# Kernel tuning notes

Measured on AMD Instinct MI355X. Metric: run time of the kernel, lower is better.

Reference implementation:

```python
import jax, jax.numpy as jnp
import numpy as np

B, S, D = 4, 1024, 1024
H, HD = 16, 64
MAXPOS = 1024  # max_position_embeddings


def setup_inputs() -> dict:
    key = jax.random.key(0)
    ks = jax.random.split(key, 10)
    sc = 0.02
    return {
        "hidden_states": jax.random.normal(ks[0], (B, S, D), dtype=jnp.float32),
        "attention_mask": jnp.zeros((B, 1, 1, S), dtype=jnp.float32),
        "across_attention_prior": jax.random.uniform(ks[1], (B, H, S, S), dtype=jnp.float32),
        "head_mask": jnp.ones((1, H, 1, 1), dtype=jnp.float32),
        "Wq": jax.random.normal(ks[2], (D, D), dtype=jnp.float32) * sc,
        "bq": jnp.zeros((D,), dtype=jnp.float32),
        "Wk": jax.random.normal(ks[3], (D, D), dtype=jnp.float32) * sc,
        "bk": jnp.zeros((D,), dtype=jnp.float32),
        "Wv": jax.random.normal(ks[4], (D, D), dtype=jnp.float32) * sc,
        "bv": jnp.zeros((D,), dtype=jnp.float32),
        "dist_emb": jax.random.normal(ks[5], (2 * MAXPOS - 1, HD), dtype=jnp.float32) * sc,
    }


def _heads(x):
    # [B,S,D] -> [B,H,S,HD]
    return x.reshape(B, S, H, HD).transpose(0, 2, 1, 3)


def reference(hidden_states, attention_mask, across_attention_prior, head_mask,
              Wq, bq, Wk, bk, Wv, bv, dist_emb):
    q = _heads(hidden_states @ Wq + bq)  # [B,H,S,HD]
    k = _heads(hidden_states @ Wk + bk)
    v = _heads(hidden_states @ Wv + bv)

    scores = jnp.einsum("bhld,bhrd->bhlr", q, k)

    # relative_key_query positional bias
    pos = jnp.arange(S)
    distance = pos[:, None] - pos[None, :]  # [S,S]
    pe = dist_emb[distance + MAXPOS - 1]  # [S,S,HD] (l, r, d)
    scores = scores + jnp.einsum("bhld,lrd->bhlr", q, pe)
    scores = scores + jnp.einsum("bhrd,lrd->bhlr", k, pe)

    scores = scores / jnp.sqrt(jnp.float32(HD))
    scores = scores + attention_mask  # additive mask, broadcast [B,1,1,S]

    probs = jax.nn.softmax(scores, axis=-1)
    probs = probs * across_attention_prior  # post-softmax multiplicative prior
    probs = probs * head_mask  # dropout prob = 0 (eval)

    ctx = jnp.einsum("bhlr,bhrd->bhld", probs, v)
    ctx = ctx.transpose(0, 2, 1, 3).reshape(B, S, D)
    return ctx
```

## Files before the change

kernel.cpp:

```cpp
#include <hip/hip_runtime.h>


typedef unsigned short u16;
typedef unsigned int   u32;
typedef unsigned long long u64;
typedef __attribute__((ext_vector_type(8))) short bfx8;
typedef __attribute__((ext_vector_type(4))) float f32x4;

#define MFMA_BF16(a, b, c) __builtin_amdgcn_mfma_f32_16x16x32_bf16(a, b, c, 0, 0, 0)

__device__ __forceinline__ u16 f2bf(float f) {
    union { float f; u32 u; } c; c.f = f;
    u32 u = c.u;
    return (u16)((u + 0x7FFFu + ((u >> 16) & 1u)) >> 16);
}
__device__ __forceinline__ float bf2f(u16 v) {
    union { u32 u; float f; } c; c.u = ((u32)v) << 16;
    return c.f;
}
__device__ __forceinline__ float load_f(const void* p, long i, bool bf) {
    return bf ? bf2f(((const u16*)p)[i]) : ((const float*)p)[i];
}
__device__ __forceinline__ u16 load_bf(const void* p, long i, bool bf) {
    return bf ? ((const u16*)p)[i] : f2bf(((const float*)p)[i]);
}

__device__ __forceinline__ void gload16(const u16* g, u16* l) {
    __builtin_amdgcn_global_load_lds(
        (__attribute__((address_space(1))) void*)g,
        (__attribute__((address_space(3))) void*)l, 16, 0, 0);
}

__device__ __forceinline__ bfx8 ld_sw(const u16* arr, int row, int chunk) {
    return *(const bfx8*)(arr + row * 64 + ((chunk ^ (row & 7)) * 8));
}

__global__ void k_detect(const u32* hid, int* flags) {
    __shared__ int cnt;
    if (threadIdx.x == 0) cnt = 0;
    __syncthreads();
    int c = 0;
    for (int i = threadIdx.x; i < 1024; i += 256) {
        u32 w = hid[i];
        u32 e = (w >> 7) & 0xFFu;
        if (e >= 100u && e <= 140u) c++;
    }
    atomicAdd(&cnt, c);
    __syncthreads();
    if (threadIdx.x == 0) flags[0] = (cnt > 512) ? 1 : 0;
}

__global__ void k_prep(const void* hidden, const void* dist, const void* mask,
                       const void* hm, const void* bq, const void* bk,
                       const void* bv, const int* flags, u16* hid_bf,
                       u16* dist_bf, float* mask_f, float* hm_f, float* bias_f) {
    const bool bf = flags[0] != 0;
    const long NH = 4L * 1024 * 1024, ND = 2047L * 64, NM = 4096, NB = 3072, NHM = 16;
    const long TOT = NH + ND + NM + NB + NHM;
    for (long i = (long)blockIdx.x * 256 + threadIdx.x; i < TOT;
         i += (long)gridDim.x * 256) {
        if (i < NH) hid_bf[i] = load_bf(hidden, i, bf);
        else if (i < NH + ND) dist_bf[i - NH] = load_bf(dist, i - NH, bf);
        else if (i < NH + ND + NM) mask_f[i - NH - ND] = load_f(mask, i - NH - ND, bf);
        else if (i < NH + ND + NM + NB) {
            long j = i - NH - ND - NM;
            const void* src = (j < 1024) ? bq : ((j < 2048) ? bk : bv);
            bias_f[j] = load_f(src, j & 1023, bf);
        } else {
            long j = i - NH - ND - NM - NB;
            hm_f[j] = load_f(hm, j, bf);
        }
    }
}

__global__ void k_transpose(const void* Wq, const void* Wk, const void* Wv,
                            const int* flags, u16* wt) {
    const bool bf = flags[0] != 0;
    __shared__ float t[32][33];
    const int z = blockIdx.z;
    const void* W = (z == 0) ? Wq : ((z == 1) ? Wk : Wv);
    int x = blockIdx.x * 32 + threadIdx.x;
    for (int i = 0; i < 4; i++) {
        int y = blockIdx.y * 32 + threadIdx.y + i * 8;
        t[threadIdx.y + i * 8][threadIdx.x] = load_f(W, (long)y * 1024 + x, bf);
    }
    __syncthreads();
    int x2 = blockIdx.y * 32 + threadIdx.x;
    u16* out = wt + (long)z * 1024 * 1024;
    for (int i = 0; i < 4; i++) {
        int y2 = blockIdx.x * 32 + threadIdx.y + i * 8;
        out[(long)y2 * 1024 + x2] = f2bf(t[threadIdx.x][threadIdx.y + i * 8]);
    }
}

__global__ __launch_bounds__(256, 2)
void k_qkv_gemm(const u16* A, const u16* Bt, const float* bias,
                u16* qb, u16* kb, u16* vb) {
    __shared__ u16 sA[128 * 32];
    __shared__ u16 sB[128 * 32];
    const int tid = threadIdx.x;
    const int w = tid >> 6, lane = tid & 63;
    const int quad = lane >> 4, nl = lane & 15;
    const int wr = w >> 1, wc = w & 1;
    const int n0 = blockIdx.x * 128, m0 = blockIdx.y * 128;

    f32x4 acc[4][4];
#pragma unroll
    for (int a = 0; a < 4; a++)
#pragma unroll
        for (int b = 0; b < 4; b++) acc[a][b] = (f32x4){0.f, 0.f, 0.f, 0.f};

    for (int kt = 0; kt < 32; kt++) {
        const int k0 = kt * 32;
        __syncthreads();
#pragma unroll
        for (int j = 0; j < 2; j++) {
            int row = 32 * w + 16 * j + (lane >> 2);
            int seg = lane & 3;
            gload16(A + (long)(m0 + row) * 1024 + k0 + seg * 8, sA + 1024 * w + 512 * j);
            gload16(Bt + (long)(n0 + row) * 1024 + k0 + seg * 8, sB + 1024 * w + 512 * j);
        }
        __syncthreads();

        bfx8 af[4], bfr[4];
#pragma unroll
        for (int f = 0; f < 4; f++) {
            af[f]  = *(const bfx8*)(sA + (64 * wr + 16 * f + nl) * 32 + quad * 8);
            bfr[f] = *(const bfx8*)(sB + (64 * wc + 16 * f + nl) * 32 + quad * 8);
        }
#pragma unroll
        for (int fm = 0; fm < 4; fm++)
#pragma unroll
            for (int fn = 0; fn < 4; fn++)
                acc[fm][fn] = MFMA_BF16(af[fm], bfr[fn], acc[fm][fn]);
    }

#pragma unroll
    for (int fm = 0; fm < 4; fm++) {
#pragma unroll
        for (int fn = 0; fn < 4; fn++) {
            int n = n0 + 64 * wc + 16 * fn + nl;
            int which = n >> 10, hcol = n & 1023;
            int h = hcol >> 6, hd = hcol & 63;
            float bias_v = bias[n];
            int mbase = m0 + 64 * wr + 16 * fm + 4 * quad;
            int b = mbase >> 10, s = mbase & 1023;
            if (which == 2) {
                u64 pk = 0;
#pragma unroll
                for (int reg = 0; reg < 4; reg++)
                    pk |= (u64)f2bf(acc[fm][fn][reg] + bias_v) << (16 * reg);
                *(u64*)&vb[((long)((b * 16 + h) * 64 + hd)) * 1024 + s] = pk;
            } else {
                u16* op = (which == 0) ? qb : kb;
#pragma unroll
                for (int reg = 0; reg < 4; reg++)
                    op[((long)((b * 16 + h) * 1024 + s + reg)) * 64 + hd] =
                        f2bf(acc[fm][fn][reg] + bias_v);
            }
        }
    }
}

__global__ __launch_bounds__(256, 3)
void k_attn(const u16* qb, const u16* kb, const u16* vTb, const u16* Eb,
            const float* maskf, const float* hmf, const void* prior,
            const int* flags, void* out) {
    __shared__ __align__(16) u16 smem[24576];
    u16* sK  = smem;
    u16* sVT = smem + 4096;
    u16* sE  = smem + 8192;
    u16* sP  = smem + 8192;
    u16* sDk = smem + 16384;

    const int tid = threadIdx.x;
    const int w = tid >> 6, lane = tid & 63;
    const int quad = lane >> 4, nl = lane & 15;
    const int rloc = lane >> 3;
    const int cperm = (lane & 7) ^ rloc;
    const int bh = blockIdx.x, b = bh >> 4, h = bh & 15;
    const int l0 = blockIdx.y * 64;
    const bool bf = flags[0] != 0;

    const u16* qbh = qb  + (long)bh * 65536;
    const u16* kbh = kb  + (long)bh * 65536;
    const u16* vbh = vTb + (long)bh * 65536;

    const bfx8 aq0 = *(const bfx8*)(qbh + (l0 + 16 * w + nl) * 64 + quad * 8);
    const bfx8 aq1 = *(const bfx8*)(qbh + (l0 + 16 * w + nl) * 64 + quad * 8 + 32);

    f32x4 accv[4];
#pragma unroll
    for (int f = 0; f < 4; f++) accv[f] = (f32x4){0.f, 0.f, 0.f, 0.f};
    float zacc[4] = {0.f, 0.f, 0.f, 0.f};
    const int jb_base = l0 + 960;

    for (int it = 0; it < 16; it++) {
        const int r0 = it * 64;
        __syncthreads();

        const int jb = jb_base - r0;
#pragma unroll
        for (int j = 0; j < 2; j++) {
            int row = 16 * w + 8 * j + rloc;
            gload16(kbh + (r0 + row) * 64 + cperm * 8, sK + (16 * w + 8 * j) * 64);
            gload16(vbh + row * 1024 + r0 + cperm * 8, sVT + (16 * w + 8 * j) * 64);
        }
#pragma unroll
        for (int j = 0; j < 4; j++) {
            int row = 32 * w + 8 * j + rloc;
            int je = jb + row; if (je > 2046) je = 2046;
            gload16(Eb + je * 64 + cperm * 8, sE + (32 * w + 8 * j) * 64);
        }
        float pr[4][4], mval[4];
#pragma unroll
        for (int fn = 0; fn < 4; fn++) {
            mval[fn] = maskf[b * 1024 + r0 + fn * 16 + nl];
#pragma unroll
            for (int reg = 0; reg < 4; reg++) {
                long pidx = ((long)(bh * 1024 + l0 + 16 * w + 4 * quad + reg)) * 1024
                            + r0 + fn * 16 + nl;
                pr[fn][reg] = bf ? bf2f(((const u16*)prior)[pidx])
                                 : ((const float*)prior)[pidx];
            }
        }
        __syncthreads();

        const bfx8 ak0 = ld_sw(sK, 16 * w + nl, quad);
        const bfx8 ak1 = ld_sw(sK, 16 * w + nl, 4 + quad);
        u32 dqp[8][2];
#pragma unroll
        for (int fc = 0; fc < 8; fc++) {
            bfx8 be0 = ld_sw(sE, fc * 16 + nl, quad);
            bfx8 be1 = ld_sw(sE, fc * 16 + nl, 4 + quad);
            f32x4 dq = (f32x4){0.f, 0.f, 0.f, 0.f};
            dq = MFMA_BF16(aq0, be0, dq);
            dq = MFMA_BF16(aq1, be1, dq);
            f32x4 dk = (f32x4){0.f, 0.f, 0.f, 0.f};
            dk = MFMA_BF16(ak0, be0, dk);
            dk = MFMA_BF16(ak1, be1, dk);
            dqp[fc][0] = (u32)f2bf(dq[0]) | ((u32)f2bf(dq[1]) << 16);
            dqp[fc][1] = (u32)f2bf(dq[2]) | ((u32)f2bf(dq[3]) << 16);
            int u = fc * 16 + nl;
            u64 pk = (u64)f2bf(dk[0]) | ((u64)f2bf(dk[1]) << 16)
                   | ((u64)f2bf(dk[2]) << 32) | ((u64)f2bf(dk[3]) << 48);
            *(u64*)(sDk + u * 64 + (((4 * w + quad) ^ (u & 15)) * 4)) = pk;
        }
        f32x4 accs[4];
#pragma unroll
        for (int fn = 0; fn < 4; fn++) {
            bfx8 bk0 = ld_sw(sK, fn * 16 + nl, quad);
            bfx8 bk1 = ld_sw(sK, fn * 16 + nl, 4 + quad);
            f32x4 s = (f32x4){0.f, 0.f, 0.f, 0.f};
            s = MFMA_BF16(aq0, bk0, s);
            s = MFMA_BF16(aq1, bk1, s);
            accs[fn] = s;
        }
        __syncthreads();

#pragma unroll
        for (int reg = 0; reg < 4; reg++) {
            int srcl = quad * 16 + ((4 * quad + reg + 15 - nl) & 15);
            int bidx = srcl * 4;
            u32 bp[8];
#pragma unroll
            for (int fc = 0; fc < 8; fc++)
                bp[fc] = (u32)__builtin_amdgcn_ds_bpermute(bidx, (int)dqp[fc][reg >> 1]);
#pragma unroll
            for (int fn = 0; fn < 4; fn++) {
                int u = 16 * w + 4 * quad + reg + 63 - 16 * fn - nl;
                u32 word = bp[u >> 4];
                u16 dqv = (reg & 1) ? (u16)(word >> 16) : (u16)word;
                int ri = 16 * fn + nl;
                u16 dkv = sDk[u * 64 + (((ri >> 2) ^ (u & 15)) * 4) + (ri & 3)];
                float s = (accs[fn][reg] + bf2f(dqv) + bf2f(dkv)) * 0.125f + mval[fn];
                float e = __expf(s);
                zacc[reg] += e;
                int li = 16 * w + 4 * quad + reg, ci = fn * 16 + nl;
                sP[li * 64 + (((ci >> 3) ^ (li & 7)) * 8) + (ci & 7)] =
                    f2bf(e * pr[fn][reg]);
            }
        }
        bfx8 ap0 = ld_sw(sP, 16 * w + nl, quad);
        bfx8 ap1 = ld_sw(sP, 16 * w + nl, 4 + quad);
#pragma unroll
        for (int fd = 0; fd < 4; fd++) {
            bfx8 bv0 = ld_sw(sVT, fd * 16 + nl, quad);
            bfx8 bv1 = ld_sw(sVT, fd * 16 + nl, 4 + quad);
            accv[fd] = MFMA_BF16(ap0, bv0, accv[fd]);
            accv[fd] = MFMA_BF16(ap1, bv1, accv[fd]);
        }
    }

#pragma unroll
    for (int reg = 0; reg < 4; reg++) {
        float z = zacc[reg];
        z += __shfl_xor(z, 1);
        z += __shfl_xor(z, 2);
        z += __shfl_xor(z, 4);
        z += __shfl_xor(z, 8);
        zacc[reg] = z;
    }
    const float hm = hmf[h];
#pragma unroll
    for (int fd = 0; fd < 4; fd++) {
#pragma unroll
        for (int reg = 0; reg < 4; reg++) {
            int l = l0 + 16 * w + 4 * quad + reg;
            int d = fd * 16 + nl;
            float val = accv[fd][reg] * hm / zacc[reg];
            long oidx = ((long)(b * 1024 + l)) * 1024 + h * 64 + d;
            if (bf) ((u16*)out)[oidx] = f2bf(val);
            else    ((float*)out)[oidx] = val;
        }
    }
}

extern "C" void kernel_launch(void* const* d_in, const int* in_sizes, int n_in,
                              void* d_out, int out_size, void* d_ws, size_t ws_size,
                              hipStream_t stream) {
    char* ws = (char*)d_ws;
    int*   flags   = (int*)ws;
    u16*   hid_bf  = (u16*)(ws + 256);
    u16*   wt_bf   = (u16*)(ws + 8388864);
    u16*   dist_bf = (u16*)(ws + 14680320);
    float* mask_f  = (float*)(ws + 14942464);
    float* bias_f  = (float*)(ws + 14958848);
    float* hm_f    = (float*)(ws + 14971136);
    u16*   q_bf    = (u16*)(ws + 14971392);
    u16*   k_bf    = (u16*)(ws + 23360000);
    u16*   v_bf    = (u16*)(ws + 31748608);

    k_detect<<<1, 256, 0, stream>>>((const u32*)d_in[0], flags);
    k_prep<<<2048, 256, 0, stream>>>(d_in[0], d_in[10], d_in[1], d_in[3],
                                     d_in[5], d_in[7], d_in[9], flags,
                                     hid_bf, dist_bf, mask_f, hm_f, bias_f);
    k_transpose<<<dim3(32, 32, 3), dim3(32, 8), 0, stream>>>(
        d_in[4], d_in[6], d_in[8], flags, wt_bf);
    k_qkv_gemm<<<dim3(24, 32), 256, 0, stream>>>(hid_bf, wt_bf, bias_f,
                                                 q_bf, k_bf, v_bf);
    k_attn<<<dim3(64, 16), 256, 0, stream>>>(q_bf, k_bf, v_bf, dist_bf,
                                             mask_f, hm_f, d_in[2], flags, d_out);
}
```

Baseline: 560.5 us.

## Compute only needed relative-position diagonals and store skewed bias in padded LDS

Each wave now computes only the 5 of 8 E-tile column blocks its rows actually touch for the q·E and k·E relative-position products, rather than all 8. Results are scattered directly into padded (stride 68) skewed LDS buffers indexed by relative offset, which replaces the ds_bpermute shuffles and the XOR-swizzled dk store. The probability tile P now uses a padded stride-72 layout instead of a swizzle. The aim is fewer MFMAs and less cross-lane data movement, at the cost of scalar 16-bit LDS scatter writes with branches, possible bank conflicts, and a slightly larger LDS footprint.

```diff
diff --git a/kernel.cpp b/kernel.cpp
--- a/kernel.cpp
+++ b/kernel.cpp
@@ -166,12 +166,13 @@
 void k_attn(const u16* qb, const u16* kb, const u16* vTb, const u16* Eb,
             const float* maskf, const float* hmf, const void* prior,
             const int* flags, void* out) {
-    __shared__ __align__(16) u16 smem[24576];
+    __shared__ __align__(16) u16 smem[25088];
     u16* sK  = smem;
     u16* sVT = smem + 4096;
     u16* sE  = smem + 8192;
     u16* sP  = smem + 8192;
-    u16* sDk = smem + 16384;
+    u16* bqB = smem + 16384;
+    u16* bkB = smem + 20736;
 
     const int tid = threadIdx.x;
     const int w = tid >> 6, lane = tid & 63;
@@ -195,6 +196,10 @@
     float zacc[4] = {0.f, 0.f, 0.f, 0.f};
     const int jb_base = l0 + 960;
 
+    const int lpb   = 16 * w + 4 * quad;
+    const int bqrd  = lpb * 68 + 63 - nl;
+    const int bkrd  = lpb * 68 + nl;
+
     for (int it = 0; it < 16; it++) {
         const int r0 = it * 64;
         __syncthreads();
@@ -209,7 +214,9 @@
 #pragma unroll
         for (int j = 0; j < 4; j++) {
             int row = 32 * w + 8 * j + rloc;
-            int je = jb + row; if (je > 2046) je = 2046;
+            int je = jb + row;
+            if (je > 2046) je = 2046;
+            if (je < 0) je = 0;
             gload16(Eb + je * 64 + cperm * 8, sE + (32 * w + 8 * j) * 64);
         }
         float pr[4][4], mval[4];
@@ -228,23 +235,35 @@
 
         const bfx8 ak0 = ld_sw(sK, 16 * w + nl, quad);
         const bfx8 ak1 = ld_sw(sK, 16 * w + nl, 4 + quad);
-        u32 dqp[8][2];
-#pragma unroll
-        for (int fc = 0; fc < 8; fc++) {
+#pragma unroll
+        for (int d = 0; d < 5; d++) {
+            const int fc = w + d;
             bfx8 be0 = ld_sw(sE, fc * 16 + nl, quad);
             bfx8 be1 = ld_sw(sE, fc * 16 + nl, 4 + quad);
             f32x4 dq = (f32x4){0.f, 0.f, 0.f, 0.f};
             dq = MFMA_BF16(aq0, be0, dq);
             dq = MFMA_BF16(aq1, be1, dq);
+#pragma unroll
+            for (int reg = 0; reg < 4; reg++) {
+                int lp = lpb + reg;
+                int t = 16 * fc + nl - lp;
+                if (t >= 0 && t < 64) bqB[lp * 68 + t] = f2bf(dq[reg]);
+            }
+        }
+#pragma unroll
+        for (int d = 0; d < 5; d++) {
+            const int fc = 3 - w + d;
+            bfx8 be0 = ld_sw(sE, fc * 16 + nl, quad);
+            bfx8 be1 = ld_sw(sE, fc * 16 + nl, 4 + quad);
             f32x4 dk = (f32x4){0.f, 0.f, 0.f, 0.f};
             dk = MFMA_BF16(ak0, be0, dk);
             dk = MFMA_BF16(ak1, be1, dk);
-            dqp[fc][0] = (u32)f2bf(dq[0]) | ((u32)f2bf(dq[1]) << 16);
-            dqp[fc][1] = (u32)f2bf(dq[2]) | ((u32)f2bf(dq[3]) << 16);
-            int u = fc * 16 + nl;
-            u64 pk = (u64)f2bf(dk[0]) | ((u64)f2bf(dk[1]) << 16)
-                   | ((u64)f2bf(dk[2]) << 32) | ((u64)f2bf(dk[3]) << 48);
-            *(u64*)(sDk + u * 64 + (((4 * w + quad) ^ (u & 15)) * 4)) = pk;
+#pragma unroll
+            for (int reg = 0; reg < 4; reg++) {
+                int rp = lpb + reg;
+                int row = 16 * fc + nl + rp - 63;
+                if (row >= 0 && row < 64) bkB[row * 68 + rp] = f2bf(dk[reg]);
+            }
         }
         f32x4 accs[4];
 #pragma unroll
@@ -259,30 +278,19 @@
         __syncthreads();
 
 #pragma unroll
-        for (int reg = 0; reg < 4; reg++) {
-            int srcl = quad * 16 + ((4 * quad + reg + 15 - nl) & 15);
-            int bidx = srcl * 4;
-            u32 bp[8];
-#pragma unroll
-            for (int fc = 0; fc < 8; fc++)
-                bp[fc] = (u32)__builtin_amdgcn_ds_bpermute(bidx, (int)dqp[fc][reg >> 1]);
-#pragma unroll
-            for (int fn = 0; fn < 4; fn++) {
-                int u = 16 * w + 4 * quad + reg + 63 - 16 * fn - nl;
-                u32 word = bp[u >> 4];
-                u16 dqv = (reg & 1) ? (u16)(word >> 16) : (u16)word;
-                int ri = 16 * fn + nl;
-                u16 dkv = sDk[u * 64 + (((ri >> 2) ^ (u & 15)) * 4) + (ri & 3)];
-                float s = (accs[fn][reg] + bf2f(dqv) + bf2f(dkv)) * 0.125f + mval[fn];
+        for (int fn = 0; fn < 4; fn++) {
+#pragma unroll
+            for (int reg = 0; reg < 4; reg++) {
+                float dqv = bf2f(bqB[bqrd + reg * 68 - fn * 16]);
+                float dkv = bf2f(bkB[bkrd + reg * 68 + fn * 16]);
+                float s = (accs[fn][reg] + dqv + dkv) * 0.125f + mval[fn];
                 float e = __expf(s);
                 zacc[reg] += e;
-                int li = 16 * w + 4 * quad + reg, ci = fn * 16 + nl;
-                sP[li * 64 + (((ci >> 3) ^ (li & 7)) * 8) + (ci & 7)] =
-                    f2bf(e * pr[fn][reg]);
-            }
-        }
-        bfx8 ap0 = ld_sw(sP, 16 * w + nl, quad);
-        bfx8 ap1 = ld_sw(sP, 16 * w + nl, 4 + quad);
+                sP[(lpb + reg) * 72 + fn * 16 + nl] = f2bf(e * pr[fn][reg]);
+            }
+        }
+        bfx8 ap0 = *(const bfx8*)(sP + (16 * w + nl) * 72 + quad * 8);
+        bfx8 ap1 = *(const bfx8*)(sP + (16 * w + nl) * 72 + quad * 8 + 32);
 #pragma unroll
         for (int fd = 0; fd < 4; fd++) {
             bfx8 bv0 = ld_sw(sVT, fd * 16 + nl, quad);
```

Result: faster. 521.9 us (-6.9%).
